# Optimization experiments

Measured on AMD Instinct MI355X. Metric: run time of the kernel, lower is better.

## Reference

```python
import jax, jax.numpy as jnp
import numpy as np

N_NODES = 50000
EMB = 256
HEADS = 2
N_BASE_EDGES = 100000


def setup_inputs() -> dict:
    key = jax.random.key(0)
    ks = jax.random.split(key, 12)
    x = jax.random.normal(ks[0], (N_NODES, EMB), dtype=jnp.float32)
    # bipartite edges: sources in left half, targets in right half -> no self-loops
    src = jax.random.randint(ks[1], (N_BASE_EDGES,), 0, N_NODES // 2)
    dst = jax.random.randint(ks[2], (N_BASE_EDGES,), N_NODES // 2, N_NODES)
    edge_index = jnp.stack([src, dst]).astype(jnp.int64)
    hd = EMB // HEADS
    s = 0.02
    params = {
        "Wkqv": jax.random.normal(ks[3], (EMB, 3 * EMB), dtype=jnp.float32) * s,
        "bkqv": jnp.zeros((3 * EMB,), dtype=jnp.float32),
        "W1": jax.random.normal(ks[4], (2 * hd, hd), dtype=jnp.float32) * s,
        "b1": jnp.zeros((hd,), dtype=jnp.float32),
        "W2": jax.random.normal(ks[5], (hd, 1), dtype=jnp.float32) * s,
        "b2": jnp.zeros((1,), dtype=jnp.float32),
        "Wout": jax.random.normal(ks[6], (EMB, EMB), dtype=jnp.float32) * s,
        "bout": jnp.zeros((EMB,), dtype=jnp.float32),
    }
    return {"x": x, "edge_index": edge_index, **params}


def reference(x, edge_index, Wkqv, bkqv, W1, b1, W2, b2, Wout, bout):
    N, emb = x.shape
    H = HEADS
    hd = emb // H
    # MetaGNNNoEdgeAttr.forward preprocessing: make undirected + self loops.
    # Input is bipartite (no self-loops), so remove_self_loops is a no-op.
    ei = jnp.concatenate([edge_index, edge_index[::-1]], axis=1)
    loops = jnp.arange(N, dtype=edge_index.dtype)
    src = jnp.concatenate([ei[0], loops])  # j (message source)
    dst = jnp.concatenate([ei[1], loops])  # i (message target / softmax index)

    # single GNN layer (n_layers=1)
    kqv = x @ Wkqv + bkqv  # [N, 3*emb]
    q = kqv[dst, :emb].reshape(-1, H, hd)                                  # [E,H,hd]
    k = kqv[src, emb:2 * emb].reshape(-1, H, hd) / jnp.sqrt(jnp.float32(hd))
    v = kqv[src, 2 * emb:].reshape(-1, H, hd)

    h = jax.nn.relu(jnp.concatenate([k, q], axis=-1) @ W1 + b1)  # [E,H,hd]
    a = (h @ W2 + b2).squeeze(-1)                                # [E,H]

    # segment softmax over destination nodes (every node has a self-loop)
    m = jax.ops.segment_max(a, dst, num_segments=N)              # [N,H]
    ex = jnp.exp(a - m[dst])
    s = jax.ops.segment_sum(ex, dst, num_segments=N)             # [N,H]
    alpha = ex / (s[dst] + 1e-16)                                # [E,H]

    msg = (alpha[..., None] * v).reshape(-1, emb) @ Wout + bout  # [E,emb]
    out = jax.ops.segment_sum(msg, dst, num_segments=N)          # [N,emb]
    return jax.nn.relu(out) + x
```

## Files before the change

kernel.cpp:

```cpp
#include <hip/hip_runtime.h>
#include <hip/hip_bf16.h>

#define EMB 256

typedef __bf16 bf16_t;
typedef __attribute__((ext_vector_type(8))) __bf16 bf16x8;
typedef __attribute__((ext_vector_type(4))) __bf16 bf16x4;
typedef __attribute__((ext_vector_type(4))) float floatx4;

__device__ __forceinline__ int eidx(const int* __restrict__ p, int is64, long long k){
  return is64 ? p[2*k] : p[(int)k];
}
__device__ __forceinline__ void async_load16(const void* g, void* l){
  __builtin_amdgcn_global_load_lds(
      (const __attribute__((address_space(1))) unsigned int*)g,
      (__attribute__((address_space(3))) unsigned int*)l,
      16, 0, 0);
}
__device__ __forceinline__ float4 cvt4(bf16x4 v){
  return make_float4((float)v.x, (float)v.y, (float)v.z, (float)v.w);
}
__device__ __forceinline__ int detect64(const int* __restrict__ ei){
  return ((ei[1] | ei[3] | ei[5] | ei[7]) == 0) ? 1 : 0;
}

__global__ void cvt_x_kernel(const float* __restrict__ x, bf16_t* __restrict__ xb, int n4){
  int t = blockIdx.x*blockDim.x + threadIdx.x;
  if (t >= n4) return;
  const float4 v = *(const float4*)(x + (size_t)t*4);
  bf16x4 o = { (bf16_t)v.x, (bf16_t)v.y, (bf16_t)v.z, (bf16_t)v.w };
  *(bf16x4*)(xb + (size_t)t*4) = o;
}

__global__ void prep_weights(const float* __restrict__ Wkqv, const float* __restrict__ bkqv,
                             const float* __restrict__ W1,
                             bf16_t* __restrict__ WcombT, float* __restrict__ bcomb){
  int n = blockIdx.x * blockDim.x + threadIdx.x;
  int c = blockIdx.y;
  if (n >= 768) return;
  const float rs = rsqrtf(128.0f);
  bool isBias = (c == 256);
  const float* arow = isBias ? bkqv : (Wkqv + (size_t)c*768);
  float val;
  if (n < 256){
    int h = n >> 7, d = n & 127;
    float s = 0.f;
    for (int t = 0; t < 128; ++t)
      s = fmaf(arow[h*128 + t], W1[(size_t)(128 + t)*128 + d], s);
    val = s;
  } else {
    int r = n - 256;
    int h = r >> 8, t8 = r & 255;
    int g = t8 >> 3, half = (t8 >> 2) & 1, dd = t8 & 3;
    int d = g*4 + dd;
    if (half == 0){
      float s = 0.f;
      for (int t = 0; t < 128; ++t)
        s = fmaf(arow[256 + h*128 + t], W1[(size_t)t*128 + d], s);
      val = s * rs;
    } else {
      val = arow[512 + h*128 + d];
    }
  }
  if (isBias) bcomb[n] = val;
  else        WcombT[(size_t)n*256 + c] = (bf16_t)val;
}

__global__ void prep_wout(const float* __restrict__ W, bf16_t* __restrict__ Wt){
  int t = blockIdx.x*blockDim.x + threadIdx.x;
  int n = t & 255, c = t >> 8;
  Wt[(size_t)n*256 + c] = (bf16_t)W[(size_t)c*256 + n];
}

__global__ void deg_kernel(const int* __restrict__ ei,
                           int* __restrict__ deg, int E0, int Nn){
  int t = blockIdx.x*blockDim.x + threadIdx.x;
  if (t >= 2*E0) return;
  int is64 = detect64(ei);
  int i = (t < E0) ? eidx(ei,is64,(long long)E0+t) : eidx(ei,is64,t-E0);
  i = min(max(i,0), Nn-1);
  atomicAdd(deg + i, 1);
}

__global__ __launch_bounds__(1024) void scan1_kernel(const int* __restrict__ deg,
                                                     int* __restrict__ off,
                                                     int* __restrict__ bsum, int N){
  __shared__ int wsum[16];
  int tid = threadIdx.x, lane = tid & 63, w = tid >> 6;
  int i = blockIdx.x*1024 + tid;
  int v = (i < N) ? (deg[i] + 1) : 0;
  int incl = v;
  #pragma unroll
  for (int o = 1; o < 64; o <<= 1){
    int t = __shfl_up(incl, o, 64);
    if (lane >= o) incl += t;
  }
  if (lane == 63) wsum[w] = incl;
  __syncthreads();
  if (w == 0 && lane < 16){
    int sv = wsum[lane];
    #pragma unroll
    for (int o = 1; o < 16; o <<= 1){
      int t = __shfl_up(sv, o, 64);
      if (lane >= o) sv += t;
    }
    wsum[lane] = sv;
  }
  __syncthreads();
  int wpref = (w == 0) ? 0 : wsum[w-1];
  if (i < N) off[i] = wpref + incl - v;
  if (tid == 1023) bsum[blockIdx.x] = wpref + incl;
}

__global__ __launch_bounds__(1024) void scan2_kernel(int* __restrict__ bsum,
                                                     int* __restrict__ off, int nb, int N){
  __shared__ int wsum[16];
  int tid = threadIdx.x, lane = tid & 63, w = tid >> 6;
  int v = (tid < nb) ? bsum[tid] : 0;
  int incl = v;
  #pragma unroll
  for (int o = 1; o < 64; o <<= 1){
    int t = __shfl_up(incl, o, 64);
    if (lane >= o) incl += t;
  }
  if (lane == 63) wsum[w] = incl;
  __syncthreads();
  if (w == 0 && lane < 16){
    int sv = wsum[lane];
    #pragma unroll
    for (int o = 1; o < 16; o <<= 1){
      int t = __shfl_up(sv, o, 64);
      if (lane >= o) sv += t;
    }
    wsum[lane] = sv;
  }
  __syncthreads();
  int wpref = (w == 0) ? 0 : wsum[w-1];
  if (tid < nb) bsum[tid] = wpref + incl - v;
  if (tid == 1023) off[N] = wpref + incl;
}

__global__ void scan3_kernel(int* __restrict__ off, const int* __restrict__ bsum, int N){
  int i = blockIdx.x*256 + threadIdx.x;
  if (i < N) off[i] += bsum[i >> 10];
}

__global__ void scatter_kernel(const int* __restrict__ ei,
                               const int* __restrict__ off, int* __restrict__ cursor,
                               int* __restrict__ bj, int E0, int Nn){
  int e = blockIdx.x*blockDim.x + threadIdx.x;
  int E = 2*E0 + Nn;
  if (e >= E) return;
  int is64 = detect64(ei);
  int j, i;
  if (e < E0){ j = eidx(ei,is64,e); i = eidx(ei,is64,(long long)E0+e); }
  else if (e < 2*E0){ int t = e - E0; i = eidx(ei,is64,t); j = eidx(ei,is64,(long long)E0+t); }
  else { i = j = e - 2*E0; }
  i = min(max(i,0), Nn-1); j = min(max(j,0), Nn-1);
  int pos = atomicAdd(cursor + i, 1);
  bj[off[i] + pos] = j;
}

template<int MODE, int MLOOP, typename OutT>
__global__ __launch_bounds__(512, 4) void mfma_gemmB(
    const bf16_t* __restrict__ A, const bf16_t* __restrict__ Bt,
    const float* __restrict__ bias, OutT* __restrict__ C,
    int M, int N,
    const int* __restrict__ deg, const float* __restrict__ xres)
{
  __shared__ bf16_t Bs[128*256];
  const int tid = threadIdx.x;
  const int wave = tid >> 6, lane = tid & 63;
  const int row16 = lane & 15, quad = lane >> 4;
  const int n0 = blockIdx.y << 7;

  {
    const bf16_t* gsrc = Bt + (size_t)(n0 + wave*16 + row16)*256 + quad*8;
    char* ldst = (char*)Bs + wave*8192;
    #pragma unroll
    for (int kt = 0; kt < 8; ++kt)
      async_load16(gsrc + kt*32, ldst + kt*1024);
  }
  __syncthreads();

  const int wm = (wave >> 1) * 64;
  const int wn = (wave & 1) * 64;

  float4 b4[4];
  #pragma unroll
  for (int nt=0;nt<4;++nt)
    b4[nt] = *(const float4*)(bias + n0 + wn + nt*16 + quad*4);

  for (int l = 0; l < MLOOP; ++l){
    const int m0 = (blockIdx.x*MLOOP + l) << 8;
    if (m0 >= M) return;

    const bf16_t* ap[4];
    #pragma unroll
    for (int t = 0; t < 4; ++t)
      ap[t] = A + (size_t)min(m0 + wm + t*16 + row16, M-1)*256 + quad*8;

    floatx4 acc[4][4];
    #pragma unroll
    for (int a=0;a<4;++a)
      #pragma unroll
      for (int b=0;b<4;++b) acc[a][b] = (floatx4){0.f,0.f,0.f,0.f};

    #pragma unroll
    for (int kt = 0; kt < 8; ++kt){
      bf16x8 af[4], bfr[4];
      #pragma unroll
      for (int t = 0; t < 4; ++t)
        af[t]  = *(const bf16x8*)(ap[t] + kt*32);
      #pragma unroll
      for (int t = 0; t < 4; ++t)
        bfr[t] = *(const bf16x8*)((const char*)Bs + (((wn>>4)+t)*8 + kt)*1024 + lane*16);
      #pragma unroll
      for (int mt=0;mt<4;++mt)
        #pragma unroll
        for (int nt=0;nt<4;++nt)
          acc[mt][nt] = __builtin_amdgcn_mfma_f32_16x16x32_bf16(bfr[nt], af[mt], acc[mt][nt], 0,0,0);
    }

    #pragma unroll
    for (int mt=0;mt<4;++mt){
      const int m = m0 + wm + mt*16 + row16;
      if (m >= M) continue;
      const float dg = (MODE==1) ? (float)(deg[m]+1) : 0.f;
      #pragma unroll
      for (int nt=0;nt<4;++nt){
        const int nb = n0 + wn + nt*16 + quad*4;
        if (MODE == 0){
          bf16x4 o = { (bf16_t)(acc[mt][nt][0] + b4[nt].x),
                       (bf16_t)(acc[mt][nt][1] + b4[nt].y),
                       (bf16_t)(acc[mt][nt][2] + b4[nt].z),
                       (bf16_t)(acc[mt][nt][3] + b4[nt].w) };
          *(bf16x4*)((bf16_t*)C + (size_t)m*N + nb) = o;
        } else {
          const float4 xr = *(const float4*)(xres + (size_t)m*N + nb);
          float4 o;
          o.x = fmaxf(acc[mt][nt][0] + dg*b4[nt].x, 0.f) + xr.x;
          o.y = fmaxf(acc[mt][nt][1] + dg*b4[nt].y, 0.f) + xr.y;
          o.z = fmaxf(acc[mt][nt][2] + dg*b4[nt].z, 0.f) + xr.z;
          o.w = fmaxf(acc[mt][nt][3] + dg*b4[nt].w, 0.f) + xr.w;
          *(float4*)((float*)C + (size_t)m*N + nb) = o;
        }
      }
    }
  }
}

__device__ __forceinline__ float score4(bf16x8 kvv, float4 qv, float4 b1v, float4 w2v){
  return fmaxf(qv.x+(float)kvv[0]+b1v.x, 0.f)*w2v.x
       + fmaxf(qv.y+(float)kvv[1]+b1v.y, 0.f)*w2v.y
       + fmaxf(qv.z+(float)kvv[2]+b1v.z, 0.f)*w2v.z
       + fmaxf(qv.w+(float)kvv[3]+b1v.w, 0.f)*w2v.w;
}
__device__ __forceinline__ float hredux(float p){
  #pragma unroll
  for (int o = 16; o >= 1; o >>= 1)
    p += __shfl_xor(p, o, 64);
  return p;
}
__global__ __launch_bounds__(256) void fused_attn_kernel(
    const bf16_t* __restrict__ P, const int* __restrict__ bj, const int* __restrict__ off,
    const float* __restrict__ b1, const float* __restrict__ W2, const float* __restrict__ b2,
    bf16_t* __restrict__ aggb, int Nn)
{
  int i = blockIdx.x * (blockDim.x >> 6) + (threadIdx.x >> 6);
  if (i >= Nn) return;
  int lane = threadIdx.x & 63;
  int h = lane >> 5, g = lane & 31, d = g * 4;

  const float4 qv  = cvt4(*(const bf16x4*)(P + (size_t)i*768 + h*128 + d));
  const float4 b1v = *(const float4*)(b1 + d);
  const float4 w2v = *(const float4*)(W2 + d);
  const float b2v  = b2[0];
  const bf16_t* __restrict__ Pkv = P + 256 + h*256 + g*8;

  float m = -3.0e38f, s = 0.f;
  float4 acc = make_float4(0.f,0.f,0.f,0.f);
  const int s0 = off[i], s1 = off[i+1], s1m1 = s1 - 1;

  for (int t = s0; t < s1; t += 4){
    const int cnt = s1 - t;
    const int jA = bj[t];
    const int jB = bj[min(t+1, s1m1)];
    const int jC = bj[min(t+2, s1m1)];
    const int jD = bj[min(t+3, s1m1)];
    const bf16x8 kA = *(const bf16x8*)(Pkv + (size_t)jA*768);
    const bf16x8 kB = *(const bf16x8*)(Pkv + (size_t)jB*768);
    const bf16x8 kC = *(const bf16x8*)(Pkv + (size_t)jC*768);
    const bf16x8 kD = *(const bf16x8*)(Pkv + (size_t)jD*768);
    float pA = hredux(score4(kA, qv, b1v, w2v));
    float pB = hredux(score4(kB, qv, b1v, w2v));
    float pC = hredux(score4(kC, qv, b1v, w2v));
    float pD = hredux(score4(kD, qv, b1v, w2v));
    const float aA = pA + b2v;
    const float aB = (cnt > 1) ? pB + b2v : -3.0e38f;
    const float aC = (cnt > 2) ? pC + b2v : -3.0e38f;
    const float aD = (cnt > 3) ? pD + b2v : -3.0e38f;
    const float amax = fmaxf(fmaxf(aA, aB), fmaxf(aC, aD));
    const float mn = fmaxf(m, amax);
    const float sc = __expf(m - mn);
    const float eA = __expf(aA - mn);
    const float eB = __expf(aB - mn);
    const float eC = __expf(aC - mn);
    const float eD = __expf(aD - mn);
    s = s*sc + ((eA + eB) + (eC + eD));
    acc.x = acc.x*sc + ((eA*(float)kA[4] + eB*(float)kB[4]) + (eC*(float)kC[4] + eD*(float)kD[4]));
    acc.y = acc.y*sc + ((eA*(float)kA[5] + eB*(float)kB[5]) + (eC*(float)kC[5] + eD*(float)kD[5]));
    acc.z = acc.z*sc + ((eA*(float)kA[6] + eB*(float)kB[6]) + (eC*(float)kC[6] + eD*(float)kD[6]));
    acc.w = acc.w*sc + ((eA*(float)kA[7] + eB*(float)kB[7]) + (eC*(float)kC[7] + eD*(float)kD[7]));
    m = mn;
  }
  float inv = 1.f / (s + 1e-16f);
  bf16x4 ob = { (bf16_t)(acc.x*inv), (bf16_t)(acc.y*inv), (bf16_t)(acc.z*inv), (bf16_t)(acc.w*inv) };
  *(bf16x4*)(aggb + (size_t)i*256 + h*128 + d) = ob;
}

extern "C" void kernel_launch(void* const* d_in, const int* in_sizes, int n_in,
                              void* d_out, int out_size, void* d_ws, size_t ws_size,
                              hipStream_t stream)
{
  const float* x     = (const float*)d_in[0];
  const int*   ei    = (const int*)d_in[1];
  const float* Wkqv  = (const float*)d_in[2];
  const float* bkqv  = (const float*)d_in[3];
  const float* W1    = (const float*)d_in[4];
  const float* b1    = (const float*)d_in[5];
  const float* W2    = (const float*)d_in[6];
  const float* b2    = (const float*)d_in[7];
  const float* Wout  = (const float*)d_in[8];
  const float* bout  = (const float*)d_in[9];
  float* out = (float*)d_out;

  const int N  = in_sizes[0] / EMB;
  const int E0 = in_sizes[1] / 2;
  const int E  = 2*E0 + N;

  float* base = (float*)d_ws;
  bf16_t* WcombT = (bf16_t*)base;
  float*  bcomb  = base + 98304;
  bf16_t* WoutT  = (bf16_t*)(base + 98304 + 768);
  bf16_t* xb     = (bf16_t*)(base + 131840);
  bf16_t* Pb     = (bf16_t*)(base + 131840 + 6400000);
  bf16_t* aggb   = (bf16_t*)(Pb + (size_t)N*768);
  int* deg       = (int*)(aggb + (size_t)N*256);
  int* cursor    = deg + N;
  int* flag      = cursor + N;
  int* off       = flag + 1;
  int* bj        = off + (N+1);
  int* bsum      = (int*)aggb;

  hipMemsetAsync(deg, 0, (size_t)2*N*sizeof(int), stream);

  cvt_x_kernel<<<((N*EMB/4)+255)/256,256,0,stream>>>(x, xb, N*EMB/4);
  prep_weights<<<dim3(3,257),256,0,stream>>>(Wkqv, bkqv, W1, WcombT, bcomb);
  prep_wout<<<256,256,0,stream>>>(Wout, WoutT);

  deg_kernel<<<(2*E0+255)/256,256,0,stream>>>(ei, deg, E0, N);
  const int nb = (N + 1023)/1024;
  scan1_kernel<<<nb,1024,0,stream>>>(deg, off, bsum, N);
  scan2_kernel<<<1,1024,0,stream>>>(bsum, off, nb, N);
  scan3_kernel<<<(N+255)/256,256,0,stream>>>(off, bsum, N);
  scatter_kernel<<<(E+255)/256,256,0,stream>>>(ei, off, cursor, bj, E0, N);

  const int nmt = (N + 255)/256;
  mfma_gemmB<0, 3, bf16_t><<<dim3((nmt+2)/3, 6),512,0,stream>>>(
      xb, WcombT, bcomb, Pb, N, 768, nullptr, nullptr);
  fused_attn_kernel<<<(N+3)/4,256,0,stream>>>(Pb, bj, off, b1, W2, b2, aggb, N);
  mfma_gemmB<1, 1, float><<<dim3(nmt, 2),512,0,stream>>>(
      aggb, WoutT, bout, out, N, 256, deg, x);
}
```

Before: 318.9 us.

## Merge prep kernels, fold scan3 into consumers, use double-buffered 256x256 GEMM tiles

Four preprocessing kernels (x conversion, weight folding, Wout transpose, degree count) are merged into one launch that dispatches on block index. The scan3 pass is removed: scatter and attention now add the block prefix bsum on the fly, so bsum moves to its own buffer instead of aliasing aggb. The GEMM becomes a 1024-thread kernel with 256x256 output tiles, A and B staged through LDS in double-buffered 64-wide K chunks, and blocks ordered in strips of 8 M-tiles. The aim is fewer launches and more data reuse per GEMM block, at the cost of heavier LDS use and lower occupancy.

```diff
diff --git a/kernel.cpp b/kernel.cpp
--- a/kernel.cpp
+++ b/kernel.cpp
@@ -24,62 +24,63 @@
   return ((ei[1] | ei[3] | ei[5] | ei[7]) == 0) ? 1 : 0;
 }
 
-__global__ void cvt_x_kernel(const float* __restrict__ x, bf16_t* __restrict__ xb, int n4){
-  int t = blockIdx.x*blockDim.x + threadIdx.x;
-  if (t >= n4) return;
-  const float4 v = *(const float4*)(x + (size_t)t*4);
-  bf16x4 o = { (bf16_t)v.x, (bf16_t)v.y, (bf16_t)v.z, (bf16_t)v.w };
-  *(bf16x4*)(xb + (size_t)t*4) = o;
-}
-
-__global__ void prep_weights(const float* __restrict__ Wkqv, const float* __restrict__ bkqv,
-                             const float* __restrict__ W1,
-                             bf16_t* __restrict__ WcombT, float* __restrict__ bcomb){
-  int n = blockIdx.x * blockDim.x + threadIdx.x;
-  int c = blockIdx.y;
-  if (n >= 768) return;
-  const float rs = rsqrtf(128.0f);
-  bool isBias = (c == 256);
-  const float* arow = isBias ? bkqv : (Wkqv + (size_t)c*768);
-  float val;
-  if (n < 256){
-    int h = n >> 7, d = n & 127;
-    float s = 0.f;
-    for (int t = 0; t < 128; ++t)
-      s = fmaf(arow[h*128 + t], W1[(size_t)(128 + t)*128 + d], s);
-    val = s;
+__global__ __launch_bounds__(256) void prep_all_kernel(
+    const float* __restrict__ x, bf16_t* __restrict__ xb, int n4,
+    const float* __restrict__ Wkqv, const float* __restrict__ bkqv,
+    const float* __restrict__ W1, bf16_t* __restrict__ WcombT, float* __restrict__ bcomb,
+    const float* __restrict__ Wout, bf16_t* __restrict__ WoutT,
+    const int* __restrict__ ei, int* __restrict__ deg, int E0, int Nn,
+    int G_CVT, int G_PW, int G_WO)
+{
+  const int bid = blockIdx.x, tid = threadIdx.x;
+  if (bid < G_CVT){
+    int t = bid*256 + tid;
+    if (t >= n4) return;
+    const float4 v = *(const float4*)(x + (size_t)t*4);
+    bf16x4 o = { (bf16_t)v.x, (bf16_t)v.y, (bf16_t)v.z, (bf16_t)v.w };
+    *(bf16x4*)(xb + (size_t)t*4) = o;
+  } else if (bid < G_CVT + G_PW){
+    int b2 = bid - G_CVT;
+    int c  = b2 / 3;
+    int n  = (b2 % 3)*256 + tid;
+    const float rs = rsqrtf(128.0f);
+    bool isBias = (c == 256);
+    const float* arow = isBias ? bkqv : (Wkqv + (size_t)c*768);
+    float val;
+    if (n < 256){
+      int h = n >> 7, d = n & 127;
+      float s = 0.f;
+      for (int t2 = 0; t2 < 128; ++t2)
+        s = fmaf(arow[h*128 + t2], W1[(size_t)(128 + t2)*128 + d], s);
+      val = s;
+    } else {
+      int r = n - 256;
+      int h = r >> 8, t8 = r & 255;
+      int g = t8 >> 3, half = (t8 >> 2) & 1, dd = t8 & 3;
+      int d = g*4 + dd;
+      if (half == 0){
+        float s = 0.f;
+        for (int t2 = 0; t2 < 128; ++t2)
+          s = fmaf(arow[256 + h*128 + t2], W1[(size_t)t2*128 + d], s);
+        val = s * rs;
+      } else {
+        val = arow[512 + h*128 + d];
+      }
+    }
+    if (isBias) bcomb[n] = val;
+    else        WcombT[(size_t)n*256 + c] = (bf16_t)val;
+  } else if (bid < G_CVT + G_PW + G_WO){
+    int t = (bid - G_CVT - G_PW)*256 + tid;
+    int n = t & 255, c = t >> 8;
+    WoutT[(size_t)n*256 + c] = (bf16_t)Wout[(size_t)c*256 + n];
   } else {
-    int r = n - 256;
-    int h = r >> 8, t8 = r & 255;
-    int g = t8 >> 3, half = (t8 >> 2) & 1, dd = t8 & 3;
-    int d = g*4 + dd;
-    if (half == 0){
-      float s = 0.f;
-      for (int t = 0; t < 128; ++t)
-        s = fmaf(arow[256 + h*128 + t], W1[(size_t)t*128 + d], s);
-      val = s * rs;
-    } else {
-      val = arow[512 + h*128 + d];
-    }
-  }
-  if (isBias) bcomb[n] = val;
-  else        WcombT[(size_t)n*256 + c] = (bf16_t)val;
-}
-
-__global__ void prep_wout(const float* __restrict__ W, bf16_t* __restrict__ Wt){
-  int t = blockIdx.x*blockDim.x + threadIdx.x;
-  int n = t & 255, c = t >> 8;
-  Wt[(size_t)n*256 + c] = (bf16_t)W[(size_t)c*256 + n];
-}
-
-__global__ void deg_kernel(const int* __restrict__ ei,
-                           int* __restrict__ deg, int E0, int Nn){
-  int t = blockIdx.x*blockDim.x + threadIdx.x;
-  if (t >= 2*E0) return;
-  int is64 = detect64(ei);
-  int i = (t < E0) ? eidx(ei,is64,(long long)E0+t) : eidx(ei,is64,t-E0);
-  i = min(max(i,0), Nn-1);
-  atomicAdd(deg + i, 1);
+    int t = (bid - G_CVT - G_PW - G_WO)*256 + tid;
+    if (t >= 2*E0) return;
+    int is64 = detect64(ei);
+    int i = (t < E0) ? eidx(ei,is64,(long long)E0+t) : eidx(ei,is64,t-E0);
+    i = min(max(i,0), Nn-1);
+    atomicAdd(deg + i, 1);
+  }
 }
 
 __global__ __launch_bounds__(1024) void scan1_kernel(const int* __restrict__ deg,
@@ -140,13 +141,9 @@
   if (tid == 1023) off[N] = wpref + incl;
 }
 
-__global__ void scan3_kernel(int* __restrict__ off, const int* __restrict__ bsum, int N){
-  int i = blockIdx.x*256 + threadIdx.x;
-  if (i < N) off[i] += bsum[i >> 10];
-}
-
 __global__ void scatter_kernel(const int* __restrict__ ei,
-                               const int* __restrict__ off, int* __restrict__ cursor,
+                               const int* __restrict__ off, const int* __restrict__ bsum,
+                               int* __restrict__ cursor,
                                int* __restrict__ bj, int E0, int Nn){
   int e = blockIdx.x*blockDim.x + threadIdx.x;
   int E = 2*E0 + Nn;
@@ -158,93 +155,102 @@
   else { i = j = e - 2*E0; }
   i = min(max(i,0), Nn-1); j = min(max(j,0), Nn-1);
   int pos = atomicAdd(cursor + i, 1);
-  bj[off[i] + pos] = j;
-}
-
-template<int MODE, int MLOOP, typename OutT>
-__global__ __launch_bounds__(512, 4) void mfma_gemmB(
+  bj[off[i] + bsum[i>>10] + pos] = j;
+}
+
+template<int MODE, typename OutT>
+__global__ __launch_bounds__(1024, 4) void mfma_gemm256T(
     const bf16_t* __restrict__ A, const bf16_t* __restrict__ Bt,
     const float* __restrict__ bias, OutT* __restrict__ C,
     int M, int N,
     const int* __restrict__ deg, const float* __restrict__ xres)
 {
-  __shared__ bf16_t Bs[128*256];
+  __shared__ bf16_t As[2][256*64];
+  __shared__ bf16_t Bs[2][256*64];
   const int tid = threadIdx.x;
   const int wave = tid >> 6, lane = tid & 63;
   const int row16 = lane & 15, quad = lane >> 4;
-  const int n0 = blockIdx.y << 7;
-
-  {
-    const bf16_t* gsrc = Bt + (size_t)(n0 + wave*16 + row16)*256 + quad*8;
-    char* ldst = (char*)Bs + wave*8192;
-    #pragma unroll
-    for (int kt = 0; kt < 8; ++kt)
-      async_load16(gsrc + kt*32, ldst + kt*1024);
-  }
-  __syncthreads();
-
-  const int wm = (wave >> 1) * 64;
-  const int wn = (wave & 1) * 64;
-
-  float4 b4[4];
-  #pragma unroll
-  for (int nt=0;nt<4;++nt)
-    b4[nt] = *(const float4*)(bias + n0 + wn + nt*16 + quad*4);
-
-  for (int l = 0; l < MLOOP; ++l){
-    const int m0 = (blockIdx.x*MLOOP + l) << 8;
-    if (m0 >= M) return;
-
-    const bf16_t* ap[4];
-    #pragma unroll
-    for (int t = 0; t < 4; ++t)
-      ap[t] = A + (size_t)min(m0 + wm + t*16 + row16, M-1)*256 + quad*8;
-
-    floatx4 acc[4][4];
-    #pragma unroll
-    for (int a=0;a<4;++a)
-      #pragma unroll
-      for (int b=0;b<4;++b) acc[a][b] = (floatx4){0.f,0.f,0.f,0.f};
-
-    #pragma unroll
-    for (int kt = 0; kt < 8; ++kt){
+
+  const int nn = N >> 8;
+  const int bid = blockIdx.x;
+  const int strip = bid / (8*nn);
+  const int inner = bid % (8*nn);
+  const int m0 = (strip*8 + (inner & 7)) * 256;
+  const int n0 = (inner >> 3) * 256;
+  const int wm  = (wave >> 2) * 64;
+  const int wnq = (wave & 3) * 64;
+
+  const int gm0 = min(m0 + wave*16 + row16, M-1);
+  const int gn0 = n0 + wave*16 + row16;
+  const bf16_t* gA = A  + (size_t)gm0*256 + quad*8;
+  const bf16_t* gB = Bt + (size_t)gn0*256 + quad*8;
+
+  #define STAGE64(buf, kb) do{ \
+    async_load16(gA + (kb),      (char*)As[buf] + (wave*2+0)*1024); \
+    async_load16(gA + (kb) + 32, (char*)As[buf] + (wave*2+1)*1024); \
+    async_load16(gB + (kb),      (char*)Bs[buf] + (wave*2+0)*1024); \
+    async_load16(gB + (kb) + 32, (char*)Bs[buf] + (wave*2+1)*1024); }while(0)
+
+  STAGE64(0, 0);
+
+  floatx4 acc[4][4];
+  #pragma unroll
+  for (int a=0;a<4;++a)
+    #pragma unroll
+    for (int b=0;b<4;++b) acc[a][b] = (floatx4){0.f,0.f,0.f,0.f};
+
+  #pragma unroll
+  for (int kt = 0; kt < 4; ++kt){
+    const int cur = kt & 1, nxt = cur ^ 1;
+
+    __syncthreads();
+
+    if (kt < 3) STAGE64(nxt, (kt+1)*64);
+
+    #pragma unroll
+    for (int kk = 0; kk < 2; ++kk){
       bf16x8 af[4], bfr[4];
       #pragma unroll
-      for (int t = 0; t < 4; ++t)
-        af[t]  = *(const bf16x8*)(ap[t] + kt*32);
-      #pragma unroll
-      for (int t = 0; t < 4; ++t)
-        bfr[t] = *(const bf16x8*)((const char*)Bs + (((wn>>4)+t)*8 + kt)*1024 + lane*16);
+      for (int t = 0; t < 4; ++t){
+        af[t]  = *(const bf16x8*)((const char*)As[cur] + (((wm>>4)+t)*2 + kk)*1024 + lane*16);
+        bfr[t] = *(const bf16x8*)((const char*)Bs[cur] + (((wnq>>4)+t)*2 + kk)*1024 + lane*16);
+      }
       #pragma unroll
       for (int mt=0;mt<4;++mt)
         #pragma unroll
         for (int nt=0;nt<4;++nt)
           acc[mt][nt] = __builtin_amdgcn_mfma_f32_16x16x32_bf16(bfr[nt], af[mt], acc[mt][nt], 0,0,0);
     }
-
-    #pragma unroll
-    for (int mt=0;mt<4;++mt){
-      const int m = m0 + wm + mt*16 + row16;
-      if (m >= M) continue;
-      const float dg = (MODE==1) ? (float)(deg[m]+1) : 0.f;
-      #pragma unroll
-      for (int nt=0;nt<4;++nt){
-        const int nb = n0 + wn + nt*16 + quad*4;
-        if (MODE == 0){
-          bf16x4 o = { (bf16_t)(acc[mt][nt][0] + b4[nt].x),
-                       (bf16_t)(acc[mt][nt][1] + b4[nt].y),
-                       (bf16_t)(acc[mt][nt][2] + b4[nt].z),
-                       (bf16_t)(acc[mt][nt][3] + b4[nt].w) };
-          *(bf16x4*)((bf16_t*)C + (size_t)m*N + nb) = o;
-        } else {
-          const float4 xr = *(const float4*)(xres + (size_t)m*N + nb);
-          float4 o;
-          o.x = fmaxf(acc[mt][nt][0] + dg*b4[nt].x, 0.f) + xr.x;
-          o.y = fmaxf(acc[mt][nt][1] + dg*b4[nt].y, 0.f) + xr.y;
-          o.z = fmaxf(acc[mt][nt][2] + dg*b4[nt].z, 0.f) + xr.z;
-          o.w = fmaxf(acc[mt][nt][3] + dg*b4[nt].w, 0.f) + xr.w;
-          *(float4*)((float*)C + (size_t)m*N + nb) = o;
-        }
+  }
+  #undef STAGE64
+
+  float4 b4[4];
+  #pragma unroll
+  for (int nt=0;nt<4;++nt)
+    b4[nt] = *(const float4*)(bias + n0 + wnq + nt*16 + quad*4);
+
+  #pragma unroll
+  for (int mt=0;mt<4;++mt){
+    const int m = m0 + wm + mt*16 + row16;
+    if (m >= M) continue;
+    const float dg = (MODE==1) ? (float)(deg[m]+1) : 0.f;
+    #pragma unroll
+    for (int nt=0;nt<4;++nt){
+      const int nb = n0 + wnq + nt*16 + quad*4;
+      if (MODE == 0){
+        bf16x4 o = { (bf16_t)(acc[mt][nt][0] + b4[nt].x),
+                     (bf16_t)(acc[mt][nt][1] + b4[nt].y),
+                     (bf16_t)(acc[mt][nt][2] + b4[nt].z),
+                     (bf16_t)(acc[mt][nt][3] + b4[nt].w) };
+        *(bf16x4*)((bf16_t*)C + (size_t)m*N + nb) = o;
+      } else {
+        const float4 xr = *(const float4*)(xres + (size_t)m*N + nb);
+        float4 o;
+        o.x = fmaxf(acc[mt][nt][0] + dg*b4[nt].x, 0.f) + xr.x;
+        o.y = fmaxf(acc[mt][nt][1] + dg*b4[nt].y, 0.f) + xr.y;
+        o.z = fmaxf(acc[mt][nt][2] + dg*b4[nt].z, 0.f) + xr.z;
+        o.w = fmaxf(acc[mt][nt][3] + dg*b4[nt].w, 0.f) + xr.w;
+        *(float4*)((float*)C + (size_t)m*N + nb) = o;
       }
     }
   }
@@ -264,6 +270,7 @@
 }
 __global__ __launch_bounds__(256) void fused_attn_kernel(
     const bf16_t* __restrict__ P, const int* __restrict__ bj, const int* __restrict__ off,
+    const int* __restrict__ bsum,
     const float* __restrict__ b1, const float* __restrict__ W2, const float* __restrict__ b2,
     bf16_t* __restrict__ aggb, int Nn)
 {
@@ -280,7 +287,9 @@
 
   float m = -3.0e38f, s = 0.f;
   float4 acc = make_float4(0.f,0.f,0.f,0.f);
-  const int s0 = off[i], s1 = off[i+1], s1m1 = s1 - 1;
+  const int s0 = off[i] + bsum[i>>10];
+  const int s1 = (i+1 < Nn) ? off[i+1] + bsum[(i+1)>>10] : off[Nn];
+  const int s1m1 = s1 - 1;
 
   for (int t = s0; t < s1; t += 4){
     const int cnt = s1 - t;
@@ -351,25 +360,28 @@
   int* flag      = cursor + N;
   int* off       = flag + 1;
   int* bj        = off + (N+1);
-  int* bsum      = (int*)aggb;
+  int* bsum      = bj + E;
 
   hipMemsetAsync(deg, 0, (size_t)2*N*sizeof(int), stream);
 
-  cvt_x_kernel<<<((N*EMB/4)+255)/256,256,0,stream>>>(x, xb, N*EMB/4);
-  prep_weights<<<dim3(3,257),256,0,stream>>>(Wkqv, bkqv, W1, WcombT, bcomb);
-  prep_wout<<<256,256,0,stream>>>(Wout, WoutT);
-
-  deg_kernel<<<(2*E0+255)/256,256,0,stream>>>(ei, deg, E0, N);
+  const int n4 = N*EMB/4;
+  const int G_CVT = (n4 + 255)/256;
+  const int G_PW  = 3*257;
+  const int G_WO  = 256;
+  const int G_DEG = (2*E0 + 255)/256;
+  prep_all_kernel<<<G_CVT+G_PW+G_WO+G_DEG,256,0,stream>>>(
+      x, xb, n4, Wkqv, bkqv, W1, WcombT, bcomb, Wout, WoutT, ei, deg, E0, N,
+      G_CVT, G_PW, G_WO);
+
   const int nb = (N + 1023)/1024;
   scan1_kernel<<<nb,1024,0,stream>>>(deg, off, bsum, N);
   scan2_kernel<<<1,1024,0,stream>>>(bsum, off, nb, N);
-  scan3_kernel<<<(N+255)/256,256,0,stream>>>(off, bsum, N);
-  scatter_kernel<<<(E+255)/256,256,0,stream>>>(ei, off, cursor, bj, E0, N);
-
-  const int nmt = (N + 255)/256;
-  mfma_gemmB<0, 3, bf16_t><<<dim3((nmt+2)/3, 6),512,0,stream>>>(
+  scatter_kernel<<<(E+255)/256,256,0,stream>>>(ei, off, bsum, cursor, bj, E0, N);
+
+  const int nm256 = (((N+255)/256) + 7) & ~7;
+  mfma_gemm256T<0, bf16_t><<<nm256*3,1024,0,stream>>>(
       xb, WcombT, bcomb, Pb, N, 768, nullptr, nullptr);
-  fused_attn_kernel<<<(N+3)/4,256,0,stream>>>(Pb, bj, off, b1, W2, b2, aggb, N);
-  mfma_gemmB<1, 1, float><<<dim3(nmt, 2),512,0,stream>>>(
+  fused_attn_kernel<<<(N+3)/4,256,0,stream>>>(Pb, bj, off, bsum, b1, W2, b2, aggb, N);
+  mfma_gemm256T<1, float><<<nm256,1024,0,stream>>>(
       aggb, WoutT, bout, out, N, 256, deg, x);
 }
```

Result: faster. 279.7 us (-12.3%).
